# Kernel tuning notes

Measured on AMD Instinct MI355X. Metric: run time of the kernel, lower is better.

Reference implementation:

```python
import jax, jax.numpy as jnp
import numpy as np

B, T, D, LATENT = 256, 1000, 64, 64
H = 2 * LATENT  # GRU hidden size


def setup_inputs() -> dict:
    key = jax.random.key(0)
    ks = jax.random.split(key, 12)
    x = jax.random.normal(ks[0], (B, T, D), dtype=jnp.float32)
    tps = jnp.sort(jax.random.uniform(ks[1], (T,), dtype=jnp.float32) * 10.0)
    mask = jax.random.randint(ks[2], (B, T), 0, 2, dtype=jnp.int32)
    s_ih = 1.0 / np.sqrt(D)
    s_h = 1.0 / np.sqrt(H)
    W_ih = jax.random.normal(ks[3], (3 * H, D), dtype=jnp.float32) * s_ih
    W_hh = jax.random.normal(ks[4], (3 * H, H), dtype=jnp.float32) * s_h
    b_ih = jax.random.normal(ks[5], (3 * H,), dtype=jnp.float32) * s_h
    b_hh = jax.random.normal(ks[6], (3 * H,), dtype=jnp.float32) * s_h
    node_W1 = jax.random.normal(ks[7], (H, H), dtype=jnp.float32) * s_h
    node_b1 = jnp.zeros((H,), dtype=jnp.float32)
    node_W2 = jax.random.normal(ks[8], (H, H), dtype=jnp.float32) * s_h
    node_b2 = jnp.zeros((H,), dtype=jnp.float32)
    W_out = jax.random.normal(ks[9], (H, H), dtype=jnp.float32) * s_h
    b_out = jnp.zeros((H,), dtype=jnp.float32)
    return {"x": x, "tps": tps, "mask": mask, "W_ih": W_ih, "W_hh": W_hh,
            "b_ih": b_ih, "b_hh": b_hh, "node_W1": node_W1, "node_b1": node_b1,
            "node_W2": node_W2, "node_b2": node_b2, "W_out": W_out, "b_out": b_out}


def reference(x, tps, mask, W_ih, W_hh, b_ih, b_hh,
              node_W1, node_b1, node_W2, node_b2, W_out, b_out):
    Bb, Tt, _ = x.shape
    mf = mask.astype(x.dtype)                       # (B,T) observation mask
    # right_fill_mask: 1 wherever at least one observation occurred strictly before j
    r_fill = ((jnp.cumsum(mf, axis=1) - mf) > 0).astype(x.dtype)
    # tps prepended with tps[0]-0.01 => euler dt at step 0 is 0.01 but h_ode=h is
    # used at i==0 in the original code, so effective dt[0]=0.
    dts = jnp.concatenate([jnp.zeros((1,), x.dtype), jnp.diff(tps)])

    def step(h, inp):
        x_t, dt, m_t, r_t = inp                     # (B,D), (), (B,), (B,)
        # Neural-ODE euler step: h + dt * f(h)
        f = jnp.tanh(h @ node_W1.T + node_b1) @ node_W2.T + node_b2
        h_ode = h + dt * f
        # freeze state before first / after last observation
        h_ode = r_t[:, None] * h_ode + (1.0 - r_t[:, None]) * h
        # GRUCell (torch semantics)
        gi = x_t @ W_ih.T + b_ih
        gh = h_ode @ W_hh.T + b_hh
        ir, iz, i_n = jnp.split(gi, 3, axis=-1)
        hr, hz, h_n = jnp.split(gh, 3, axis=-1)
        r = jax.nn.sigmoid(ir + hr)
        z = jax.nn.sigmoid(iz + hz)
        n = jnp.tanh(i_n + r * h_n)
        h_rnn = (1.0 - z) * n + z * h_ode
        # mask blend: only update where observed
        h_new = m_t[:, None] * h_rnn + (1.0 - m_t[:, None]) * h_ode
        return h_new, h_new

    h0 = jnp.zeros((Bb, H), dtype=x.dtype)
    xs = (jnp.swapaxes(x, 0, 1), dts, mf.T, r_fill.T)
    _, h_arr = jax.lax.scan(step, h0, xs)           # (T,B,H)
    # last observed timestep per trajectory
    ind = Tt - 1 - jnp.argmax(mask[:, ::-1], axis=1)  # (B,)
    h_last = h_arr[ind, jnp.arange(Bb)]             # (B,H)
    return h_last @ W_out.T + b_out
```

## Files before the change

kernel.cpp:

```cpp
#include <hip/hip_runtime.h>

#define NB 256
#define NT 1000
#define ND 64
#define NH 128

typedef _Float16 h2 __attribute__((ext_vector_type(2)));

static __device__ __forceinline__ uint pk(float a, float b) {
    return __builtin_bit_cast(uint, __builtin_amdgcn_cvt_pkrtz(a, b));
}
static __device__ __forceinline__ float fdot2u(uint a, uint b, float c) {
#if __has_builtin(__builtin_amdgcn_fdot2)
    return __builtin_amdgcn_fdot2(__builtin_bit_cast(h2, a),
                                  __builtin_bit_cast(h2, b), c, false);
#else
    h2 ha = __builtin_bit_cast(h2, a), hb = __builtin_bit_cast(h2, b);
    return c + (float)ha.x * (float)hb.x + (float)ha.y * (float)hb.y;
#endif
}
static __device__ __forceinline__ float f16lo(uint u) {
    return (float)__builtin_bit_cast(h2, u).x;
}
static __device__ __forceinline__ float f16hi(uint u) {
    return (float)__builtin_bit_cast(h2, u).y;
}
static __device__ __forceinline__ float sigmoid_f(float x) {
    float e = __builtin_amdgcn_exp2f(-1.4426950408889634f * x);
    return __builtin_amdgcn_rcpf(1.0f + e);
}
static __device__ __forceinline__ float tanh_f(float x) {
    float e = __builtin_amdgcn_exp2f(-2.8853900817779268f * x);
    return 2.0f * __builtin_amdgcn_rcpf(1.0f + e) - 1.0f;
}
static __device__ __forceinline__ float qsum(float v) {
    int a = __builtin_amdgcn_update_dpp(0, __builtin_bit_cast(int, v),
                                        0xB1, 0xF, 0xF, true);
    v += __builtin_bit_cast(float, a);
    int b = __builtin_amdgcn_update_dpp(0, __builtin_bit_cast(int, v),
                                        0x4E, 0xF, 0xF, true);
    v += __builtin_bit_cast(float, b);
    return v;
}
static __device__ __forceinline__ void ld8(const float* p, uint* d) {
    const float4 A = *(const float4*)p;
    const float4 B = *(const float4*)(p + 4);
    d[0] = pk(A.x, A.y); d[1] = pk(A.z, A.w);
    d[2] = pk(B.x, B.y); d[3] = pk(B.z, B.w);
}
#define PIN(v) asm volatile("" : "+v"(v))
#define WAVEBAR() asm volatile("s_waitcnt lgkmcnt(0)\n\ts_barrier" ::: "memory")

__global__ __launch_bounds__(128) void mfuse(
    const float* __restrict__ W_hh, const float* __restrict__ nW2,
    float* __restrict__ M)
{
    __shared__ float wrow[NH];
    const int r = blockIdx.x;
    const int j = threadIdx.x;
    wrow[j] = W_hh[(size_t)r * NH + j];
    __syncthreads();
    float a0 = 0.0f, a1 = 0.0f, a2 = 0.0f, a3 = 0.0f;
#pragma unroll 8
    for (int k = 0; k < NH; k += 4) {
        a0 += wrow[k]     * nW2[(size_t)(k)     * NH + j];
        a1 += wrow[k + 1] * nW2[(size_t)(k + 1) * NH + j];
        a2 += wrow[k + 2] * nW2[(size_t)(k + 2) * NH + j];
        a3 += wrow[k + 3] * nW2[(size_t)(k + 3) * NH + j];
    }
    M[(size_t)r * NH + j] = (a0 + a1) + (a2 + a3);
}

__global__ __launch_bounds__(384) void gi_pre(
    const float* __restrict__ x,
    const float* __restrict__ W_ih,
    const float* __restrict__ b_ih,
    const float* __restrict__ b_hh,
    ushort* __restrict__ giu)
{
    __shared__ uint xt[125][32];
    const int tid = threadIdx.x;
    const int b   = blockIdx.x;
    const int t0  = blockIdx.y * 125;

    uint wr[32];
    const float* wrow = W_ih + (size_t)tid * ND;
#pragma unroll
    for (int k = 0; k < 8; ++k) ld8(wrow + k * 8, wr + k * 4);
    const float badd = (tid < 256) ? (b_ih[tid] + b_hh[tid]) : b_ih[tid];

    for (int i = tid; i < 125 * 32; i += 384) {
        const int t = i >> 5, c = i & 31;
        const float2 v = *(const float2*)(x + ((size_t)b * NT + t0 + t) * ND + c * 2);
        xt[t][c] = pk(v.x, v.y);
    }
    __syncthreads();

    for (int t = 0; t < 125; ++t) {
        const uint4* xr = (const uint4*)&xt[t][0];
        float a0 = 0.0f, a1 = 0.0f;
#pragma unroll
        for (int k4 = 0; k4 < 8; ++k4) {
            const uint4 hv = xr[k4];
            a0 = fdot2u(wr[k4 * 4 + 0], hv.x, a0);
            a1 = fdot2u(wr[k4 * 4 + 1], hv.y, a1);
            a0 = fdot2u(wr[k4 * 4 + 2], hv.z, a0);
            a1 = fdot2u(wr[k4 * 4 + 3], hv.w, a1);
        }
        giu[((size_t)(t0 + t) * NB + b) * 384 + tid] =
            __builtin_bit_cast(ushort, (_Float16)(a0 + a1 + badd));
    }
}

template<int GI>
__global__
__attribute__((amdgpu_flat_work_group_size(512, 512)))
__attribute__((amdgpu_waves_per_eu(2, 2)))
void gruode_scan(
    const float* __restrict__ x,
    const float* __restrict__ tps,
    const int*   __restrict__ mask,
    const float* __restrict__ W_ih,
    const float* __restrict__ W_hh,
    const float* __restrict__ b_ih,
    const float* __restrict__ b_hh,
    const float* __restrict__ nW1,
    const float* __restrict__ nb1,
    const float* __restrict__ nW2,
    const float* __restrict__ nb2,
    const float* __restrict__ W_out,
    const float* __restrict__ b_out,
    const float* __restrict__ Mw,
    const ushort* __restrict__ giu,
    float* __restrict__ out)
{
    __shared__ __align__(16) _Float16 sh_h[2][NH];
    __shared__ __align__(16) _Float16 sh_tmp[NH];
    __shared__ float sh_eo[NH];
    __shared__ float sh_dt[NT];
    __shared__ int   sh_m[NT];

    const int tid = threadIdx.x;
    const int j   = tid >> 2;
    const int q   = tid & 3;
    const int b   = blockIdx.x;
    const int kb  = q * 32;
    const int qb  = q * 64;

#define WSEL(i) (((i) + (q >> 1)) & 3)

    uint w1[4][4], w2[4][4], whr[4][4], whz[4][4], whn[4][4];
    uint mr[4][4], mz[4][4], mn[4][4];
#pragma unroll
    for (int i = 0; i < 4; ++i) {
        const int c = kb + (WSEL(i) << 3);
        ld8(nW1  + (size_t)(j      ) * NH + c, w1[i]);
        ld8(nW2  + (size_t)(j      ) * NH + c, w2[i]);
        ld8(W_hh + (size_t)(j      ) * NH + c, whr[i]);
        ld8(W_hh + (size_t)(j + 128) * NH + c, whz[i]);
        ld8(W_hh + (size_t)(j + 256) * NH + c, whn[i]);
        ld8(Mw   + (size_t)(j      ) * NH + c, mr[i]);
        ld8(Mw   + (size_t)(j + 128) * NH + c, mz[i]);
        ld8(Mw   + (size_t)(j + 256) * NH + c, mn[i]);
    }
    uint wir[8], wiz[8], win[8];
    if constexpr (!GI) {
        const int kbi = q * 16;
        ld8(W_ih + (size_t)(j      ) * ND + kbi,     wir);
        ld8(W_ih + (size_t)(j      ) * ND + kbi + 8, wir + 4);
        ld8(W_ih + (size_t)(j + 128) * ND + kbi,     wiz);
        ld8(W_ih + (size_t)(j + 128) * ND + kbi + 8, wiz + 4);
        ld8(W_ih + (size_t)(j + 256) * ND + kbi,     win);
        ld8(W_ih + (size_t)(j + 256) * ND + kbi + 8, win + 4);
    }
    float bb1   = nb1[j];
    float bb2   = nb2[j];
    float brz_r = b_ih[j]       + b_hh[j];
    float brz_z = b_ih[j + 128] + b_hh[j + 128];
    float bin_n = b_ih[j + 256];
    float bhn_n = b_hh[j + 256];

    float cr = 0.0f, cz = 0.0f, cn = 0.0f;
    {
        uint b2p[4];
#pragma unroll
        for (int i = 0; i < 4; ++i) {
            const int c = kb + (WSEL(i) << 3);
            ld8(nb2 + c, b2p);
#pragma unroll
            for (int k = 0; k < 4; ++k) {
                cr = fdot2u(whr[i][k], b2p[k], cr);
                cz = fdot2u(whz[i][k], b2p[k], cz);
                cn = fdot2u(whn[i][k], b2p[k], cn);
            }
        }
        cr = qsum(cr); cz = qsum(cz); cn = qsum(cn);
    }

#pragma unroll
    for (int i = 0; i < 4; ++i)
#pragma unroll
        for (int k = 0; k < 4; ++k) {
            PIN(w1[i][k]); PIN(w2[i][k]);
            PIN(whr[i][k]); PIN(whz[i][k]); PIN(whn[i][k]);
            PIN(mr[i][k]); PIN(mz[i][k]); PIN(mn[i][k]);
        }
    PIN(bb1); PIN(bb2); PIN(bhn_n);
    PIN(cr); PIN(cz); PIN(cn);

    for (int s = tid; s < NT; s += 512) {
        sh_dt[s] = (s == 0) ? 0.0f : (tps[s] - tps[s - 1]);
        sh_m[s]  = mask[b * NT + s];
    }
    if (tid < NH) sh_h[0][tid] = (_Float16)0.0f;
    __syncthreads();

    float hj = 0.0f, hlast = 0.0f;
    int   seen = 0;

    const size_t GSTR = (size_t)NB * 384;
    const ushort* gb = giu + (size_t)b * 384 + j;
    ushort c_r, c_z, c_n, n_r, n_z, n_n;
    const float* xbase = x + (size_t)b * NT * ND + q * 16;
    float4 xc0, xc1, xc2, xc3;
    if constexpr (GI) {
        c_r = gb[0];           c_z = gb[128];           c_n = gb[256];
        n_r = gb[GSTR];        n_z = gb[GSTR + 128];    n_n = gb[GSTR + 256];
    } else {
        xc0 = *(const float4*)(xbase);
        xc1 = *(const float4*)(xbase + 4);
        xc2 = *(const float4*)(xbase + 8);
        xc3 = *(const float4*)(xbase + 12);
    }
    float dtc = sh_dt[0];
    int   mc  = sh_m[0];

    for (int s = 0; s < NT; ++s) {
        const int cur = s & 1, nxt = cur ^ 1;

        ushort p_r, p_z, p_n;
        float4 xn0, xn1, xn2, xn3;
        if constexpr (GI) {
            const int sp = (s + 2 < NT) ? (s + 2) : (NT - 1);
            const ushort* g2 = gb + (size_t)sp * GSTR;
            p_r = g2[0]; p_z = g2[128]; p_n = g2[256];
        } else {
            const int sn_ = (s + 1 < NT) ? (s + 1) : s;
            const float* xr = xbase + (size_t)sn_ * ND;
            xn0 = *(const float4*)(xr);
            xn1 = *(const float4*)(xr + 4);
            xn2 = *(const float4*)(xr + 8);
            xn3 = *(const float4*)(xr + 12);
        }
        const int sn = (s + 1 < NT) ? (s + 1) : s;
        const float dt_n = sh_dt[sn];
        const int   m_n  = sh_m[sn];

        const int   m   = mc;
        const float dte = seen ? dtc : 0.0f;

        float grf, gzf, gnf;
        if constexpr (GI) {
            grf = (float)__builtin_bit_cast(_Float16, c_r);
            gzf = (float)__builtin_bit_cast(_Float16, c_z);
            gnf = (float)__builtin_bit_cast(_Float16, c_n);
        } else {
            uint xh[8];
            xh[0] = pk(xc0.x, xc0.y); xh[1] = pk(xc0.z, xc0.w);
            xh[2] = pk(xc1.x, xc1.y); xh[3] = pk(xc1.z, xc1.w);
            xh[4] = pk(xc2.x, xc2.y); xh[5] = pk(xc2.z, xc2.w);
            xh[6] = pk(xc3.x, xc3.y); xh[7] = pk(xc3.z, xc3.w);
            grf = gzf = gnf = 0.0f;
            if (m) {
#pragma unroll
                for (int k = 0; k < 8; ++k) {
                    grf = fdot2u(wir[k], xh[k], grf);
                    gzf = fdot2u(wiz[k], xh[k], gzf);
                    gnf = fdot2u(win[k], xh[k], gnf);
                }
            }
        }

        float a1 = 0.0f, ahr = 0.0f, ahz = 0.0f, ahn = 0.0f;
        const char* hb = (const char*)&sh_h[cur][0];
        if (m) {
#pragma unroll
            for (int i = 0; i < 4; ++i) {
                const uint4 hv = *(const uint4*)(hb + qb + WSEL(i) * 16);
                a1  = fdot2u(w1[i][0],  hv.x, a1);  a1  = fdot2u(w1[i][1],  hv.y, a1);
                a1  = fdot2u(w1[i][2],  hv.z, a1);  a1  = fdot2u(w1[i][3],  hv.w, a1);
                ahr = fdot2u(whr[i][0], hv.x, ahr); ahr = fdot2u(whr[i][1], hv.y, ahr);
                ahr = fdot2u(whr[i][2], hv.z, ahr); ahr = fdot2u(whr[i][3], hv.w, ahr);
                ahz = fdot2u(whz[i][0], hv.x, ahz); ahz = fdot2u(whz[i][1], hv.y, ahz);
                ahz = fdot2u(whz[i][2], hv.z, ahz); ahz = fdot2u(whz[i][3], hv.w, ahz);
                ahn = fdot2u(whn[i][0], hv.x, ahn); ahn = fdot2u(whn[i][1], hv.y, ahn);
                ahn = fdot2u(whn[i][2], hv.z, ahn); ahn = fdot2u(whn[i][3], hv.w, ahn);
            }
        } else {
#pragma unroll
            for (int i = 0; i < 4; ++i) {
                const uint4 hv = *(const uint4*)(hb + qb + WSEL(i) * 16);
                a1 = fdot2u(w1[i][0], hv.x, a1); a1 = fdot2u(w1[i][1], hv.y, a1);
                a1 = fdot2u(w1[i][2], hv.z, a1); a1 = fdot2u(w1[i][3], hv.w, a1);
            }
        }
        const float a1q = qsum(a1);
        if (q == 0) sh_tmp[j] = (_Float16)tanh_f(a1q + bb1);
        WAVEBAR();

        float a2 = 0.0f, amr = 0.0f, amz = 0.0f, amn = 0.0f;
        if (m) {
#pragma unroll
            for (int i = 0; i < 4; ++i) {
                const uint4 tv = *(const uint4*)((const char*)sh_tmp + qb + WSEL(i) * 16);
                a2  = fdot2u(w2[i][0], tv.x, a2);  a2  = fdot2u(w2[i][1], tv.y, a2);
                a2  = fdot2u(w2[i][2], tv.z, a2);  a2  = fdot2u(w2[i][3], tv.w, a2);
                amr = fdot2u(mr[i][0], tv.x, amr); amr = fdot2u(mr[i][1], tv.y, amr);
                amr = fdot2u(mr[i][2], tv.z, amr); amr = fdot2u(mr[i][3], tv.w, amr);
                amz = fdot2u(mz[i][0], tv.x, amz); amz = fdot2u(mz[i][1], tv.y, amz);
                amz = fdot2u(mz[i][2], tv.z, amz); amz = fdot2u(mz[i][3], tv.w, amz);
                amn = fdot2u(mn[i][0], tv.x, amn); amn = fdot2u(mn[i][1], tv.y, amn);
                amn = fdot2u(mn[i][2], tv.z, amn); amn = fdot2u(mn[i][3], tv.w, amn);
            }
        } else {
#pragma unroll
            for (int i = 0; i < 4; ++i) {
                const uint4 tv = *(const uint4*)((const char*)sh_tmp + qb + WSEL(i) * 16);
                a2 = fdot2u(w2[i][0], tv.x, a2); a2 = fdot2u(w2[i][1], tv.y, a2);
                a2 = fdot2u(w2[i][2], tv.z, a2); a2 = fdot2u(w2[i][3], tv.w, a2);
            }
        }
        const float a2q  = qsum(a2);
        const float hode = hj + dte * (a2q + bb2);

        float hnew;
        if (m) {
            const float sr_t = qsum(ahr + dte * amr) + dte * cr;
            const float sz_t = qsum(ahz + dte * amz) + dte * cz;
            const float hn_t = qsum(ahn + dte * amn) + dte * cn;
            float r, z, n;
            if constexpr (GI) {
                r = sigmoid_f(sr_t + grf);
                z = sigmoid_f(sz_t + gzf);
                n = tanh_f(gnf + r * (hn_t + bhn_n));
            } else {
                r = sigmoid_f(sr_t + grf + brz_r);
                z = sigmoid_f(sz_t + gzf + brz_z);
                n = tanh_f(gnf + bin_n + r * (hn_t + bhn_n));
            }
            hnew  = (1.0f - z) * n + z * hode;
            hlast = hnew;
        } else {
            hnew = hode;
        }

        if (q == 0) sh_h[nxt][j] = (_Float16)hnew;
        hj = hnew;
        seen |= m;
        if constexpr (GI) { c_r = n_r; c_z = n_z; c_n = n_n; n_r = p_r; n_z = p_z; n_n = p_n; }
        else { xc0 = xn0; xc1 = xn1; xc2 = xn2; xc3 = xn3; }
        dtc = dt_n; mc = m_n;
        WAVEBAR();
    }

    if (q == 0) sh_eo[j] = hlast;
    __syncthreads();
    float ao = 0.0f;
#pragma unroll
    for (int i = 0; i < 8; ++i) {
        const int c = kb + (((i + 2 * q) & 7) << 2);
        const float4 wv = *(const float4*)(W_out + (size_t)j * NH + c);
        const float4 hv = *(const float4*)(sh_eo + c);
        ao += wv.x * hv.x + wv.y * hv.y + wv.z * hv.z + wv.w * hv.w;
    }
    ao = qsum(ao);
    if (q == 0) out[(size_t)b * NH + j] = ao + b_out[j];
}

extern "C" void kernel_launch(void* const* d_in, const int* in_sizes, int n_in,
                              void* d_out, int out_size, void* d_ws, size_t ws_size,
                              hipStream_t stream) {
    const float* x     = (const float*)d_in[0];
    const float* tps   = (const float*)d_in[1];
    const int*   mask  = (const int*)  d_in[2];
    const float* W_ih  = (const float*)d_in[3];
    const float* W_hh  = (const float*)d_in[4];
    const float* b_ih  = (const float*)d_in[5];
    const float* b_hh  = (const float*)d_in[6];
    const float* nW1   = (const float*)d_in[7];
    const float* nb1   = (const float*)d_in[8];
    const float* nW2   = (const float*)d_in[9];
    const float* nb2   = (const float*)d_in[10];
    const float* W_out = (const float*)d_in[11];
    const float* b_out = (const float*)d_in[12];
    float* out = (float*)d_out;

    const size_t M_BYTES  = (size_t)384 * NH * sizeof(float);
    const size_t GI_BYTES = (size_t)NT * NB * 384 * sizeof(ushort);
    float*  Mw  = (float*)d_ws;
    ushort* giu = (ushort*)((char*)d_ws + M_BYTES);

    mfuse<<<dim3(384), dim3(128), 0, stream>>>(W_hh, nW2, Mw);
    if (ws_size >= M_BYTES + GI_BYTES) {
        gi_pre<<<dim3(NB, 8), dim3(384), 0, stream>>>(x, W_ih, b_ih, b_hh, giu);
        gruode_scan<1><<<dim3(NB), dim3(512), 0, stream>>>(
            x, tps, mask, W_ih, W_hh, b_ih, b_hh,
            nW1, nb1, nW2, nb2, W_out, b_out, Mw, giu, out);
    } else {
        gruode_scan<0><<<dim3(NB), dim3(512), 0, stream>>>(
            x, tps, mask, W_ih, W_hh, b_ih, b_hh,
            nW1, nb1, nW2, nb2, W_out, b_out, Mw, nullptr, out);
    }
}
```

Before: 1.032 ms.

## Drop fused W_hh·W2 precompute; compute gh from materialized h_ode serially

Removes the mfuse kernel and the fused M = W_hh·nW2 weights, which let the hidden-gate products run in parallel with the ODE second layer. Instead h_ode is written to shared memory after the ODE step, and the three W_hh dot products are computed from it after an extra wave barrier. This frees 48 registers of weights per thread and one kernel launch, at the cost of a longer serial dependency chain per timestep (one more barrier and matvec phase on observed steps).

```diff
diff --git a/kernel.cpp b/kernel.cpp
--- a/kernel.cpp
+++ b/kernel.cpp
@@ -19,12 +19,6 @@
     return c + (float)ha.x * (float)hb.x + (float)ha.y * (float)hb.y;
 #endif
 }
-static __device__ __forceinline__ float f16lo(uint u) {
-    return (float)__builtin_bit_cast(h2, u).x;
-}
-static __device__ __forceinline__ float f16hi(uint u) {
-    return (float)__builtin_bit_cast(h2, u).y;
-}
 static __device__ __forceinline__ float sigmoid_f(float x) {
     float e = __builtin_amdgcn_exp2f(-1.4426950408889634f * x);
     return __builtin_amdgcn_rcpf(1.0f + e);
@@ -50,26 +44,6 @@
 }
 #define PIN(v) asm volatile("" : "+v"(v))
 #define WAVEBAR() asm volatile("s_waitcnt lgkmcnt(0)\n\ts_barrier" ::: "memory")
-
-__global__ __launch_bounds__(128) void mfuse(
-    const float* __restrict__ W_hh, const float* __restrict__ nW2,
-    float* __restrict__ M)
-{
-    __shared__ float wrow[NH];
-    const int r = blockIdx.x;
-    const int j = threadIdx.x;
-    wrow[j] = W_hh[(size_t)r * NH + j];
-    __syncthreads();
-    float a0 = 0.0f, a1 = 0.0f, a2 = 0.0f, a3 = 0.0f;
-#pragma unroll 8
-    for (int k = 0; k < NH; k += 4) {
-        a0 += wrow[k]     * nW2[(size_t)(k)     * NH + j];
-        a1 += wrow[k + 1] * nW2[(size_t)(k + 1) * NH + j];
-        a2 += wrow[k + 2] * nW2[(size_t)(k + 2) * NH + j];
-        a3 += wrow[k + 3] * nW2[(size_t)(k + 3) * NH + j];
-    }
-    M[(size_t)r * NH + j] = (a0 + a1) + (a2 + a3);
-}
 
 __global__ __launch_bounds__(384) void gi_pre(
     const float* __restrict__ x,
@@ -130,12 +104,12 @@
     const float* __restrict__ nb2,
     const float* __restrict__ W_out,
     const float* __restrict__ b_out,
-    const float* __restrict__ Mw,
     const ushort* __restrict__ giu,
     float* __restrict__ out)
 {
     __shared__ __align__(16) _Float16 sh_h[2][NH];
     __shared__ __align__(16) _Float16 sh_tmp[NH];
+    __shared__ __align__(16) _Float16 sh_ode[NH];
     __shared__ float sh_eo[NH];
     __shared__ float sh_dt[NT];
     __shared__ int   sh_m[NT];
@@ -150,7 +124,6 @@
 #define WSEL(i) (((i) + (q >> 1)) & 3)
 
     uint w1[4][4], w2[4][4], whr[4][4], whz[4][4], whn[4][4];
-    uint mr[4][4], mz[4][4], mn[4][4];
 #pragma unroll
     for (int i = 0; i < 4; ++i) {
         const int c = kb + (WSEL(i) << 3);
@@ -159,9 +132,6 @@
         ld8(W_hh + (size_t)(j      ) * NH + c, whr[i]);
         ld8(W_hh + (size_t)(j + 128) * NH + c, whz[i]);
         ld8(W_hh + (size_t)(j + 256) * NH + c, whn[i]);
-        ld8(Mw   + (size_t)(j      ) * NH + c, mr[i]);
-        ld8(Mw   + (size_t)(j + 128) * NH + c, mz[i]);
-        ld8(Mw   + (size_t)(j + 256) * NH + c, mn[i]);
     }
     uint wir[8], wiz[8], win[8];
     if constexpr (!GI) {
@@ -180,33 +150,14 @@
     float bin_n = b_ih[j + 256];
     float bhn_n = b_hh[j + 256];
 
-    float cr = 0.0f, cz = 0.0f, cn = 0.0f;
-    {
-        uint b2p[4];
-#pragma unroll
-        for (int i = 0; i < 4; ++i) {
-            const int c = kb + (WSEL(i) << 3);
-            ld8(nb2 + c, b2p);
-#pragma unroll
-            for (int k = 0; k < 4; ++k) {
-                cr = fdot2u(whr[i][k], b2p[k], cr);
-                cz = fdot2u(whz[i][k], b2p[k], cz);
-                cn = fdot2u(whn[i][k], b2p[k], cn);
-            }
-        }
-        cr = qsum(cr); cz = qsum(cz); cn = qsum(cn);
-    }
-
 #pragma unroll
     for (int i = 0; i < 4; ++i)
 #pragma unroll
         for (int k = 0; k < 4; ++k) {
             PIN(w1[i][k]); PIN(w2[i][k]);
             PIN(whr[i][k]); PIN(whz[i][k]); PIN(whn[i][k]);
-            PIN(mr[i][k]); PIN(mz[i][k]); PIN(mn[i][k]);
         }
     PIN(bb1); PIN(bb2); PIN(bhn_n);
-    PIN(cr); PIN(cz); PIN(cn);
 
     for (int s = tid; s < NT; s += 512) {
         sh_dt[s] = (s == 0) ? 0.0f : (tps[s] - tps[s - 1]);
@@ -281,14 +232,36 @@
             }
         }
 
-        float a1 = 0.0f, ahr = 0.0f, ahz = 0.0f, ahn = 0.0f;
+        float a1 = 0.0f;
         const char* hb = (const char*)&sh_h[cur][0];
+#pragma unroll
+        for (int i = 0; i < 4; ++i) {
+            const uint4 hv = *(const uint4*)(hb + qb + WSEL(i) * 16);
+            a1 = fdot2u(w1[i][0], hv.x, a1); a1 = fdot2u(w1[i][1], hv.y, a1);
+            a1 = fdot2u(w1[i][2], hv.z, a1); a1 = fdot2u(w1[i][3], hv.w, a1);
+        }
+        const float a1q = qsum(a1);
+        if (q == 0) sh_tmp[j] = (_Float16)tanh_f(a1q + bb1);
+        WAVEBAR();
+
+        float a2 = 0.0f;
+#pragma unroll
+        for (int i = 0; i < 4; ++i) {
+            const uint4 tv = *(const uint4*)((const char*)sh_tmp + qb + WSEL(i) * 16);
+            a2 = fdot2u(w2[i][0], tv.x, a2); a2 = fdot2u(w2[i][1], tv.y, a2);
+            a2 = fdot2u(w2[i][2], tv.z, a2); a2 = fdot2u(w2[i][3], tv.w, a2);
+        }
+        const float a2q  = qsum(a2);
+        const float hode = hj + dte * (a2q + bb2);
+
+        float hnew;
         if (m) {
+            if (q == 0) sh_ode[j] = (_Float16)hode;
+            WAVEBAR();
+            float ahr = 0.0f, ahz = 0.0f, ahn = 0.0f;
 #pragma unroll
             for (int i = 0; i < 4; ++i) {
-                const uint4 hv = *(const uint4*)(hb + qb + WSEL(i) * 16);
-                a1  = fdot2u(w1[i][0],  hv.x, a1);  a1  = fdot2u(w1[i][1],  hv.y, a1);
-                a1  = fdot2u(w1[i][2],  hv.z, a1);  a1  = fdot2u(w1[i][3],  hv.w, a1);
+                const uint4 hv = *(const uint4*)((const char*)sh_ode + qb + WSEL(i) * 16);
                 ahr = fdot2u(whr[i][0], hv.x, ahr); ahr = fdot2u(whr[i][1], hv.y, ahr);
                 ahr = fdot2u(whr[i][2], hv.z, ahr); ahr = fdot2u(whr[i][3], hv.w, ahr);
                 ahz = fdot2u(whz[i][0], hv.x, ahz); ahz = fdot2u(whz[i][1], hv.y, ahz);
@@ -296,48 +269,9 @@
                 ahn = fdot2u(whn[i][0], hv.x, ahn); ahn = fdot2u(whn[i][1], hv.y, ahn);
                 ahn = fdot2u(whn[i][2], hv.z, ahn); ahn = fdot2u(whn[i][3], hv.w, ahn);
             }
-        } else {
-#pragma unroll
-            for (int i = 0; i < 4; ++i) {
-                const uint4 hv = *(const uint4*)(hb + qb + WSEL(i) * 16);
-                a1 = fdot2u(w1[i][0], hv.x, a1); a1 = fdot2u(w1[i][1], hv.y, a1);
-                a1 = fdot2u(w1[i][2], hv.z, a1); a1 = fdot2u(w1[i][3], hv.w, a1);
-            }
-        }
-        const float a1q = qsum(a1);
-        if (q == 0) sh_tmp[j] = (_Float16)tanh_f(a1q + bb1);
-        WAVEBAR();
-
-        float a2 = 0.0f, amr = 0.0f, amz = 0.0f, amn = 0.0f;
-        if (m) {
-#pragma unroll
-            for (int i = 0; i < 4; ++i) {
-                const uint4 tv = *(const uint4*)((const char*)sh_tmp + qb + WSEL(i) * 16);
-                a2  = fdot2u(w2[i][0], tv.x, a2);  a2  = fdot2u(w2[i][1], tv.y, a2);
-                a2  = fdot2u(w2[i][2], tv.z, a2);  a2  = fdot2u(w2[i][3], tv.w, a2);
-                amr = fdot2u(mr[i][0], tv.x, amr); amr = fdot2u(mr[i][1], tv.y, amr);
-                amr = fdot2u(mr[i][2], tv.z, amr); amr = fdot2u(mr[i][3], tv.w, amr);
-                amz = fdot2u(mz[i][0], tv.x, amz); amz = fdot2u(mz[i][1], tv.y, amz);
-                amz = fdot2u(mz[i][2], tv.z, amz); amz = fdot2u(mz[i][3], tv.w, amz);
-                amn = fdot2u(mn[i][0], tv.x, amn); amn = fdot2u(mn[i][1], tv.y, amn);
-                amn = fdot2u(mn[i][2], tv.z, amn); amn = fdot2u(mn[i][3], tv.w, amn);
-            }
-        } else {
-#pragma unroll
-            for (int i = 0; i < 4; ++i) {
-                const uint4 tv = *(const uint4*)((const char*)sh_tmp + qb + WSEL(i) * 16);
-                a2 = fdot2u(w2[i][0], tv.x, a2); a2 = fdot2u(w2[i][1], tv.y, a2);
-                a2 = fdot2u(w2[i][2], tv.z, a2); a2 = fdot2u(w2[i][3], tv.w, a2);
-            }
-        }
-        const float a2q  = qsum(a2);
-        const float hode = hj + dte * (a2q + bb2);
-
-        float hnew;
-        if (m) {
-            const float sr_t = qsum(ahr + dte * amr) + dte * cr;
-            const float sz_t = qsum(ahz + dte * amz) + dte * cz;
-            const float hn_t = qsum(ahn + dte * amn) + dte * cn;
+            const float sr_t = qsum(ahr);
+            const float sz_t = qsum(ahz);
+            const float hn_t = qsum(ahn);
             float r, z, n;
             if constexpr (GI) {
                 r = sigmoid_f(sr_t + grf);
@@ -395,20 +329,17 @@
     const float* b_out = (const float*)d_in[12];
     float* out = (float*)d_out;
 
-    const size_t M_BYTES  = (size_t)384 * NH * sizeof(float);
     const size_t GI_BYTES = (size_t)NT * NB * 384 * sizeof(ushort);
-    float*  Mw  = (float*)d_ws;
-    ushort* giu = (ushort*)((char*)d_ws + M_BYTES);
-
-    mfuse<<<dim3(384), dim3(128), 0, stream>>>(W_hh, nW2, Mw);
-    if (ws_size >= M_BYTES + GI_BYTES) {
+    ushort* giu = (ushort*)d_ws;
+
+    if (ws_size >= GI_BYTES) {
         gi_pre<<<dim3(NB, 8), dim3(384), 0, stream>>>(x, W_ih, b_ih, b_hh, giu);
         gruode_scan<1><<<dim3(NB), dim3(512), 0, stream>>>(
             x, tps, mask, W_ih, W_hh, b_ih, b_hh,
-            nW1, nb1, nW2, nb2, W_out, b_out, Mw, giu, out);
+            nW1, nb1, nW2, nb2, W_out, b_out, giu, out);
     } else {
         gruode_scan<0><<<dim3(NB), dim3(512), 0, stream>>>(
             x, tps, mask, W_ih, W_hh, b_ih, b_hh,
-            nW1, nb1, nW2, nb2, W_out, b_out, Mw, nullptr, out);
-    }
-}
+            nW1, nb1, nW2, nb2, W_out, b_out, nullptr, out);
+    }
+}
```

Result: faster. 937.7 us (-9.2%).
